# Kernel optimization log

Hardware: AMD Instinct MI355X
Metric: run time of the kernel (lower is better)

## Reference

```python
import jax, jax.numpy as jnp
import numpy as np

N = 100000
C_IN = 128
C_OUT = 128
N_EDGE_TYPE = 7
N_SAMPLES = 2
E = 700000


def setup_inputs() -> dict:
    key = jax.random.key(0)
    k1, k2, k3, k4 = jax.random.split(key, 4)
    x = jax.random.normal(k1, (N, C_IN), dtype=jnp.float32)
    col = jax.random.randint(k2, (E,), 0, N, dtype=jnp.int64)
    # per-edge slot index = row * n_edge_type + edge_type, sorted (select_k_sorted needs sorted idx)
    index_sorted = jnp.sort(jax.random.randint(k3, (E,), 0, N * N_EDGE_TYPE, dtype=jnp.int64))
    weights = jax.random.normal(k4, (N_EDGE_TYPE * C_IN, C_OUT), dtype=jnp.float32)
    return {"x": x, "col": col, "index_sorted": index_sorted, "weights": weights}


def reference(x, col, index_sorted, weights):
    n, c = x.shape
    S = n * N_EDGE_TYPE  # total (node, edge_type) slots
    # group stats over the sorted slot index (replaces unique_consecutive + counts)
    counts = jax.ops.segment_sum(jnp.ones_like(index_sorted, dtype=jnp.int32),
                                 index_sorted, num_segments=S)
    starts = jnp.cumsum(counts) - counts  # first edge position of each slot
    # Monte Carlo: sample N_SAMPLES edges (with replacement) per slot
    rel = jax.random.randint(jax.random.key(42), (S, N_SAMPLES), 0, 1 << 30, dtype=jnp.int32)
    rel = rel % jnp.maximum(counts, 1)[:, None]
    gidx = starts[:, None] + rel              # [S, k] indices into the edge list
    x_col = x[col]                            # [E, C] neighbor features
    gathered = x_col[gidx]                    # [S, k, C]
    gathered = jnp.where((counts > 0)[:, None, None], gathered, jnp.zeros((), x.dtype))
    col_data = gathered.mean(axis=1)          # [S, C]
    # self slot (edge_type = n_edge_type-1) is overwritten with the node's own feature
    self_idx = jnp.arange(n) * N_EDGE_TYPE + (N_EDGE_TYPE - 1)
    col_data = col_data.at[self_idx].set(x)
    return col_data.reshape(n, N_EDGE_TYPE * c) @ weights
```

## Files before the change

kernel.cpp:

```cpp
#include <hip/hip_runtime.h>
#include <hip/hip_bf16.h>
#include <stdint.h>

#define N_NODES 100000
#define C 128
#define NET 7
#define E_EDGES 700000
#define S_SLOTS (N_NODES * NET)
#define BM 64
#define NB_CVTX 6250
#define NB_CVTW 56
#define NB_SCAN ((E_EDGES + 255) / 256)

typedef __attribute__((ext_vector_type(8))) short short8;
typedef __attribute__((ext_vector_type(4))) float f32x4;
typedef __attribute__((ext_vector_type(4))) unsigned int uint4v;

struct TF2 { uint32_t a, b; };

__host__ __device__ constexpr uint32_t rotl32c(uint32_t v, int r) {
    return (v << r) | (v >> (32 - r));
}

__host__ __device__ constexpr TF2 threefry2x32(uint32_t k0, uint32_t k1,
                                               uint32_t x0, uint32_t x1) {
    const uint32_t ks0 = k0, ks1 = k1, ks2 = 0x1BD11BDAu ^ k0 ^ k1;
    x0 += ks0; x1 += ks1;
#define RND(r) { x0 += x1; x1 = rotl32c(x1, (r)); x1 ^= x0; }
    RND(13) RND(15) RND(26) RND(6)
    x0 += ks1; x1 += ks2 + 1u;
    RND(17) RND(29) RND(16) RND(24)
    x0 += ks2; x1 += ks0 + 2u;
    RND(13) RND(15) RND(26) RND(6)
    x0 += ks0; x1 += ks1 + 3u;
    RND(17) RND(29) RND(16) RND(24)
    x0 += ks1; x1 += ks2 + 4u;
    RND(13) RND(15) RND(26) RND(6)
    x0 += ks2; x1 += ks0 + 5u;
#undef RND
    return TF2{x0, x1};
}

constexpr TF2 K2 = threefry2x32(0u, 42u, 0u, 1u);

__device__ __forceinline__ uint32_t jax_bits32(uint32_t f) {
    TF2 o = threefry2x32(K2.a, K2.b, 0u, f);
    return o.a ^ o.b;
}

__device__ __forceinline__ unsigned short f2bf(float f) {
    uint32_t u = __float_as_uint(f);
    u += 0x7fffu + ((u >> 16) & 1u);
    return (unsigned short)(u >> 16);
}

__device__ __forceinline__ uint32_t sumpack(uint32_t a, uint32_t b) {
    float alo = __uint_as_float(a << 16);
    float ahi = __uint_as_float(a & 0xffff0000u);
    float blo = __uint_as_float(b << 16);
    float bhi = __uint_as_float(b & 0xffff0000u);
    return (__float_as_uint(ahi + bhi) & 0xffff0000u) | (__float_as_uint(alo + blo) >> 16);
}

__device__ __forceinline__ uint4v sumpack4(uint4v a, uint4v b) {
    uint4v o;
    o.x = sumpack(a.x, b.x); o.y = sumpack(a.y, b.y);
    o.z = sumpack(a.z, b.z); o.w = sumpack(a.w, b.w);
    return o;
}

__global__ __launch_bounds__(256) void prep(const float* __restrict__ x,
                                            const float* __restrict__ W,
                                            const int* __restrict__ idx,
                                            const int* __restrict__ col,
                                            unsigned short* __restrict__ xb,
                                            unsigned short* __restrict__ Wf,
                                            int2* __restrict__ pairs) {
    const int b = blockIdx.x;
    if (b < NB_CVTX) {
        int i = b * 256 + threadIdx.x;
        const float4* src = (const float4*)x + (size_t)i * 2;
        float4 a = src[0], v = src[1];
        union { unsigned short u[8]; uint4v q; } o;
        o.u[0] = f2bf(a.x); o.u[1] = f2bf(a.y); o.u[2] = f2bf(a.z); o.u[3] = f2bf(a.w);
        o.u[4] = f2bf(v.x); o.u[5] = f2bf(v.y); o.u[6] = f2bf(v.z); o.u[7] = f2bf(v.w);
        ((uint4v*)xb)[i] = o.q;
    } else if (b < NB_CVTX + NB_CVTW) {
        int t = (b - NB_CVTX) * 256 + threadIdx.x;
        int l = t & 63, ks = (t >> 6) & 3, n16 = (t >> 8) & 7, et = t >> 11;
        int n = n16 * 16 + (l & 15);
        int k0 = ks * 32 + (l >> 4) * 8;
        union { unsigned short u[8]; uint4v q; } o;
#pragma unroll
        for (int j = 0; j < 8; j++)
            o.u[j] = f2bf(0.5f * W[(size_t)(et * 128 + k0 + j) * 128 + n]);
        ((uint4v*)Wf)[t] = o.q;
    } else {
        int e = (b - NB_CVTX - NB_CVTW) * 256 + threadIdx.x;
        if (e >= E_EDGES) return;
        int s = idx[e];
        if (e > 0 && idx[e - 1] == s) return;
        if (s % NET == NET - 1) return;
        int len = 1;
        while (e + len < E_EDGES && idx[e + len] == s) ++len;
        uint32_t b0 = jax_bits32((uint32_t)s * 2u + 0u) & 0x3FFFFFFFu;
        uint32_t b1 = jax_bits32((uint32_t)s * 2u + 1u) & 0x3FFFFFFFu;
        int c0 = col[e + (int)(b0 % (uint32_t)len)];
        int c1 = col[e + (int)(b1 % (uint32_t)len)];
        pairs[s] = (c0 == c1) ? make_int2(c0 + 1, 0)
                              : make_int2(c0 + 1, c1 + 1);
    }
}

__global__ __launch_bounds__(512, 4) void fused_mfma(const unsigned short* __restrict__ xb,
                                                     const int2* __restrict__ pairs,
                                                     const unsigned short* __restrict__ Wf,
                                                     float* __restrict__ out) {
    __shared__ unsigned char Alds[2][BM * 256];
    const int tid  = threadIdx.x;
    const int nb   = blockIdx.x * BM;
    const int wave = tid >> 6, lane = tid & 63;
    const int lr   = lane & 15, lg = lane >> 4;
    const char* xbc = (const char*)xb;

    const int srow = tid >> 3;
    const int q16  = (tid & 7) * 16;
    const int arow = nb + srow;
    const int prow = (arow < N_NODES) ? arow * NET : -1;
    const int sa0  = srow * 256 + ((q16 >> 4) ^ (srow & 7)) * 16;
    const int sa1  = sa0 + 128;

    uint4v g0[3][2], g1[3][2];
    int2   pset[3];
    short8 bfr[2][4];

#define GLOAD(SET, PV) { \
    int2 p_ = (PV); pset[SET] = p_; \
    if (p_.x > 0) { \
        const char* b0_ = xbc + ((size_t)(p_.x - 1) << 8); \
        g0[SET][0] = *(const uint4v*)(b0_ + q16); \
        g0[SET][1] = *(const uint4v*)(b0_ + 128 + q16); \
        if (p_.y > 0) { \
            const char* b1_ = xbc + ((size_t)(p_.y - 1) << 8); \
            g1[SET][0] = *(const uint4v*)(b1_ + q16); \
            g1[SET][1] = *(const uint4v*)(b1_ + 128 + q16); \
        } \
    } }

#define COMBINE(SET, BUF) { \
    int2 p_ = pset[SET]; \
    uint4v v0_, v1_; \
    if (p_.x <= 0) { \
        uint4v z_ = {0u, 0u, 0u, 0u}; v0_ = z_; v1_ = z_; \
    } else if (p_.y <= 0) { \
        v0_ = g0[SET][0] + 0x00800080u;    \
        v1_ = g0[SET][1] + 0x00800080u; \
    } else { \
        v0_ = sumpack4(g0[SET][0], g1[SET][0]); \
        v1_ = sumpack4(g0[SET][1], g1[SET][1]); \
    } \
    *(uint4v*)(&Alds[BUF][sa0]) = v0_; \
    *(uint4v*)(&Alds[BUF][sa1]) = v1_; }

#define LOADB(DST, ET) { _Pragma("unroll") \
    for (int ks_ = 0; ks_ < 4; ks_++) \
        (DST)[ks_] = *(const short8*)(Wf \
            + (size_t)((((ET) * 8 + wave) * 4 + ks_) * 512) + lane * 8); }

#define BARRIER() { \
    asm volatile("s_waitcnt lgkmcnt(0)" ::: "memory"); \
    __builtin_amdgcn_s_barrier(); \
    __builtin_amdgcn_sched_barrier(0); }

    f32x4 acc[4];
#pragma unroll
    for (int i = 0; i < 4; i++) acc[i] = (f32x4)0.f;

    int2 pj[7];
#pragma unroll
    for (int j = 0; j < 6; j++)
        pj[j] = (prow >= 0) ? pairs[prow + j] : make_int2(0, 0);
    pj[6] = (prow >= 0) ? make_int2(arow + 1, 0) : make_int2(0, 0);

    GLOAD(0, pj[0])
    GLOAD(1, pj[1])
    GLOAD(2, pj[2])
    LOADB(bfr[0], 0)
    COMBINE(0, 0)
    GLOAD(0, pj[3])
    BARRIER()

#pragma unroll
    for (int et = 0; et < NET; ++et) {
        const int cur = et & 1;

        if (et + 1 < NET) LOADB(bfr[cur ^ 1], et + 1)

        if (et >= 1 && et + 3 < NET) GLOAD(et % 3, pj[et + 3])

        if (et + 1 < NET) COMBINE((et + 1) % 3, cur ^ 1)

        __builtin_amdgcn_s_setprio(1);
#pragma unroll
        for (int ks = 0; ks < 4; ks++) {
            const int coff = (((ks * 4 + lg) ^ (lr & 7)) << 4);
            short8 b_ = bfr[cur][ks];
#pragma unroll
            for (int fm = 0; fm < 4; fm++) {
                short8 a_ = *(const short8*)(&Alds[cur][(fm * 16 + lr) * 256 + coff]);
                acc[fm] = __builtin_amdgcn_mfma_f32_16x16x32_bf16(a_, b_, acc[fm], 0, 0, 0);
            }
        }
        __builtin_amdgcn_s_setprio(0);

        if (et + 1 < NET) BARRIER()
    }

#pragma unroll
    for (int fm = 0; fm < 4; fm++) {
        int row0 = nb + fm * 16 + lg * 4;
        int colo = wave * 16 + lr;
#pragma unroll
        for (int j = 0; j < 4; j++)
            if (row0 + j < N_NODES)
                out[(size_t)(row0 + j) * C + colo] = acc[fm][j];
    }
#undef GLOAD
#undef COMBINE
#undef LOADB
#undef BARRIER
}

extern "C" void kernel_launch(void* const* d_in, const int* in_sizes, int n_in,
                              void* d_out, int out_size, void* d_ws, size_t ws_size,
                              hipStream_t stream) {
    const float* x   = (const float*)d_in[0];
    const int*   col = (const int*)d_in[1];
    const int*   idx = (const int*)d_in[2];
    const float* W   = (const float*)d_in[3];
    float* out = (float*)d_out;

    int2* pairs        = (int2*)d_ws;
    unsigned short* xb = (unsigned short*)((char*)pairs + (size_t)S_SLOTS * 8);
    unsigned short* Wf = xb + (size_t)N_NODES * C;

    hipMemsetAsync(pairs, 0, (size_t)S_SLOTS * sizeof(int2), stream);
    prep<<<NB_CVTX + NB_CVTW + NB_SCAN, 256, 0, stream>>>(x, W, idx, col, xb, Wf, pairs);
    fused_mfma<<<(N_NODES + BM - 1) / BM, 512, 0, stream>>>(xb, pairs, Wf, out);
}
```

Baseline: 77.22 us.

## Drop bf16 pre-conversion of x; gather fp32 rows and convert in fused kernel

Removes the prep pass that converted x to a bf16 copy. The fused kernel now gathers fp32 neighbor rows directly and sums and packs them to bf16 in registers before storing to LDS. This saves a full read and write pass over x, about 51MB of traffic plus 25MB of bf16 writes. In exchange each gather moves twice the bytes, and the per-thread registers for prefetched rows double, which may reduce occupancy.

```diff
diff --git a/kernel.cpp b/kernel.cpp
--- a/kernel.cpp
+++ b/kernel.cpp
@@ -8,7 +8,6 @@
 #define E_EDGES 700000
 #define S_SLOTS (N_NODES * NET)
 #define BM 64
-#define NB_CVTX 6250
 #define NB_CVTW 56
 #define NB_SCAN ((E_EDGES + 255) / 256)
 
@@ -54,39 +53,33 @@
     return (unsigned short)(u >> 16);
 }
 
-__device__ __forceinline__ uint32_t sumpack(uint32_t a, uint32_t b) {
-    float alo = __uint_as_float(a << 16);
-    float ahi = __uint_as_float(a & 0xffff0000u);
-    float blo = __uint_as_float(b << 16);
-    float bhi = __uint_as_float(b & 0xffff0000u);
-    return (__float_as_uint(ahi + bhi) & 0xffff0000u) | (__float_as_uint(alo + blo) >> 16);
-}
-
-__device__ __forceinline__ uint4v sumpack4(uint4v a, uint4v b) {
+__device__ __forceinline__ uint32_t pk(float lo, float hi) {
+    return (__float_as_uint(hi) & 0xffff0000u) | (__float_as_uint(lo) >> 16);
+}
+
+__device__ __forceinline__ uint4v packsum(f32x4 a0, f32x4 a1, f32x4 b0, f32x4 b1) {
+    f32x4 s0 = a0 + b0, s1 = a1 + b1;
     uint4v o;
-    o.x = sumpack(a.x, b.x); o.y = sumpack(a.y, b.y);
-    o.z = sumpack(a.z, b.z); o.w = sumpack(a.w, b.w);
+    o.x = pk(s0.x, s0.y); o.y = pk(s0.z, s0.w);
+    o.z = pk(s1.x, s1.y); o.w = pk(s1.z, s1.w);
     return o;
 }
 
-__global__ __launch_bounds__(256) void prep(const float* __restrict__ x,
-                                            const float* __restrict__ W,
+__device__ __forceinline__ uint4v packone(f32x4 a0, f32x4 a1) {
+    uint4v o;
+    o.x = pk(a0.x, a0.y); o.y = pk(a0.z, a0.w);
+    o.z = pk(a1.x, a1.y); o.w = pk(a1.z, a1.w);
+    return o + 0x00800080u;
+}
+
+__global__ __launch_bounds__(256) void prep(const float* __restrict__ W,
                                             const int* __restrict__ idx,
                                             const int* __restrict__ col,
-                                            unsigned short* __restrict__ xb,
                                             unsigned short* __restrict__ Wf,
                                             int2* __restrict__ pairs) {
     const int b = blockIdx.x;
-    if (b < NB_CVTX) {
-        int i = b * 256 + threadIdx.x;
-        const float4* src = (const float4*)x + (size_t)i * 2;
-        float4 a = src[0], v = src[1];
-        union { unsigned short u[8]; uint4v q; } o;
-        o.u[0] = f2bf(a.x); o.u[1] = f2bf(a.y); o.u[2] = f2bf(a.z); o.u[3] = f2bf(a.w);
-        o.u[4] = f2bf(v.x); o.u[5] = f2bf(v.y); o.u[6] = f2bf(v.z); o.u[7] = f2bf(v.w);
-        ((uint4v*)xb)[i] = o.q;
-    } else if (b < NB_CVTX + NB_CVTW) {
-        int t = (b - NB_CVTX) * 256 + threadIdx.x;
+    if (b < NB_CVTW) {
+        int t = b * 256 + threadIdx.x;
         int l = t & 63, ks = (t >> 6) & 3, n16 = (t >> 8) & 7, et = t >> 11;
         int n = n16 * 16 + (l & 15);
         int k0 = ks * 32 + (l >> 4) * 8;
@@ -96,7 +89,7 @@
             o.u[j] = f2bf(0.5f * W[(size_t)(et * 128 + k0 + j) * 128 + n]);
         ((uint4v*)Wf)[t] = o.q;
     } else {
-        int e = (b - NB_CVTX - NB_CVTW) * 256 + threadIdx.x;
+        int e = (b - NB_CVTW) * 256 + threadIdx.x;
         if (e >= E_EDGES) return;
         int s = idx[e];
         if (e > 0 && idx[e - 1] == s) return;
@@ -112,7 +105,7 @@
     }
 }
 
-__global__ __launch_bounds__(512, 4) void fused_mfma(const unsigned short* __restrict__ xb,
+__global__ __launch_bounds__(512, 4) void fused_mfma(const float* __restrict__ x,
                                                      const int2* __restrict__ pairs,
                                                      const unsigned short* __restrict__ Wf,
                                                      float* __restrict__ out) {
@@ -121,29 +114,33 @@
     const int nb   = blockIdx.x * BM;
     const int wave = tid >> 6, lane = tid & 63;
     const int lr   = lane & 15, lg = lane >> 4;
-    const char* xbc = (const char*)xb;
+    const char* xfc = (const char*)x;
 
     const int srow = tid >> 3;
-    const int q16  = (tid & 7) * 16;
+    const int q32  = (tid & 7) * 32;
     const int arow = nb + srow;
     const int prow = (arow < N_NODES) ? arow * NET : -1;
-    const int sa0  = srow * 256 + ((q16 >> 4) ^ (srow & 7)) * 16;
+    const int sa0  = srow * 256 + (((tid & 7)) ^ (srow & 7)) * 16;
     const int sa1  = sa0 + 128;
 
-    uint4v g0[3][2], g1[3][2];
+    f32x4 g0[3][4], g1[3][4];
     int2   pset[3];
     short8 bfr[2][4];
 
 #define GLOAD(SET, PV) { \
     int2 p_ = (PV); pset[SET] = p_; \
     if (p_.x > 0) { \
-        const char* b0_ = xbc + ((size_t)(p_.x - 1) << 8); \
-        g0[SET][0] = *(const uint4v*)(b0_ + q16); \
-        g0[SET][1] = *(const uint4v*)(b0_ + 128 + q16); \
+        const char* b0_ = xfc + ((size_t)(p_.x - 1) << 9) + q32; \
+        g0[SET][0] = *(const f32x4*)(b0_); \
+        g0[SET][1] = *(const f32x4*)(b0_ + 16); \
+        g0[SET][2] = *(const f32x4*)(b0_ + 256); \
+        g0[SET][3] = *(const f32x4*)(b0_ + 272); \
         if (p_.y > 0) { \
-            const char* b1_ = xbc + ((size_t)(p_.y - 1) << 8); \
-            g1[SET][0] = *(const uint4v*)(b1_ + q16); \
-            g1[SET][1] = *(const uint4v*)(b1_ + 128 + q16); \
+            const char* b1_ = xfc + ((size_t)(p_.y - 1) << 9) + q32; \
+            g1[SET][0] = *(const f32x4*)(b1_); \
+            g1[SET][1] = *(const f32x4*)(b1_ + 16); \
+            g1[SET][2] = *(const f32x4*)(b1_ + 256); \
+            g1[SET][3] = *(const f32x4*)(b1_ + 272); \
         } \
     } }
 
@@ -153,11 +150,11 @@
     if (p_.x <= 0) { \
         uint4v z_ = {0u, 0u, 0u, 0u}; v0_ = z_; v1_ = z_; \
     } else if (p_.y <= 0) { \
-        v0_ = g0[SET][0] + 0x00800080u;    \
-        v1_ = g0[SET][1] + 0x00800080u; \
+        v0_ = packone(g0[SET][0], g0[SET][1]); \
+        v1_ = packone(g0[SET][2], g0[SET][3]); \
     } else { \
-        v0_ = sumpack4(g0[SET][0], g1[SET][0]); \
-        v1_ = sumpack4(g0[SET][1], g1[SET][1]); \
+        v0_ = packsum(g0[SET][0], g0[SET][1], g1[SET][0], g1[SET][1]); \
+        v1_ = packsum(g0[SET][2], g0[SET][3], g1[SET][2], g1[SET][3]); \
     } \
     *(uint4v*)(&Alds[BUF][sa0]) = v0_; \
     *(uint4v*)(&Alds[BUF][sa1]) = v1_; }
@@ -241,10 +238,9 @@
     float* out = (float*)d_out;
 
     int2* pairs        = (int2*)d_ws;
-    unsigned short* xb = (unsigned short*)((char*)pairs + (size_t)S_SLOTS * 8);
-    unsigned short* Wf = xb + (size_t)N_NODES * C;
+    unsigned short* Wf = (unsigned short*)((char*)pairs + (size_t)S_SLOTS * 8);
 
     hipMemsetAsync(pairs, 0, (size_t)S_SLOTS * sizeof(int2), stream);
-    prep<<<NB_CVTX + NB_CVTW + NB_SCAN, 256, 0, stream>>>(x, W, idx, col, xb, Wf, pairs);
-    fused_mfma<<<(N_NODES + BM - 1) / BM, 512, 0, stream>>>(xb, pairs, Wf, out);
-}
+    prep<<<NB_CVTW + NB_SCAN, 256, 0, stream>>>(W, idx, col, Wf, pairs);
+    fused_mfma<<<(N_NODES + BM - 1) / BM, 512, 0, stream>>>(x, pairs, Wf, out);
+}
```

Measured after the change: 179.6 us. 133% more time.

## Shrink row tile to 32 with 256-thread blocks and per-wave 2x2 MFMA tiles

Applied to the files above, without the earlier changes.

Halves the block row tile to 32 nodes and the block to 4 waves, each wave now computing a 32x32 output tile (2 row x 2 column fragments) instead of 64x16. Weight fragments are loaded inside the compute loop per edge type rather than double-buffered one stage ahead, which lowers register use so more blocks fit per CU. The goal is more resident blocks and smaller LDS per block to hide gather latency, at the cost of twice as many blocks, more weight reloads per output row, and no prefetch of B fragments.

```diff
diff --git a/kernel.cpp b/kernel.cpp
--- a/kernel.cpp
+++ b/kernel.cpp
@@ -7,7 +7,7 @@
 #define NET 7
 #define E_EDGES 700000
 #define S_SLOTS (N_NODES * NET)
-#define BM 64
+#define BM 32
 #define NB_CVTX 6250
 #define NB_CVTW 56
 #define NB_SCAN ((E_EDGES + 255) / 256)
@@ -112,7 +112,7 @@
     }
 }
 
-__global__ __launch_bounds__(512, 4) void fused_mfma(const unsigned short* __restrict__ xb,
+__global__ __launch_bounds__(256, 8) void fused_mfma(const unsigned short* __restrict__ xb,
                                                      const int2* __restrict__ pairs,
                                                      const unsigned short* __restrict__ Wf,
                                                      float* __restrict__ out) {
@@ -132,7 +132,6 @@
 
     uint4v g0[3][2], g1[3][2];
     int2   pset[3];
-    short8 bfr[2][4];
 
 #define GLOAD(SET, PV) { \
     int2 p_ = (PV); pset[SET] = p_; \
@@ -162,19 +161,16 @@
     *(uint4v*)(&Alds[BUF][sa0]) = v0_; \
     *(uint4v*)(&Alds[BUF][sa1]) = v1_; }
 
-#define LOADB(DST, ET) { _Pragma("unroll") \
-    for (int ks_ = 0; ks_ < 4; ks_++) \
-        (DST)[ks_] = *(const short8*)(Wf \
-            + (size_t)((((ET) * 8 + wave) * 4 + ks_) * 512) + lane * 8); }
-
 #define BARRIER() { \
     asm volatile("s_waitcnt lgkmcnt(0)" ::: "memory"); \
     __builtin_amdgcn_s_barrier(); \
     __builtin_amdgcn_sched_barrier(0); }
 
-    f32x4 acc[4];
-#pragma unroll
-    for (int i = 0; i < 4; i++) acc[i] = (f32x4)0.f;
+    f32x4 acc[2][2];
+#pragma unroll
+    for (int i = 0; i < 2; i++)
+#pragma unroll
+        for (int j = 0; j < 2; j++) acc[i][j] = (f32x4)0.f;
 
     int2 pj[7];
 #pragma unroll
@@ -185,7 +181,6 @@
     GLOAD(0, pj[0])
     GLOAD(1, pj[1])
     GLOAD(2, pj[2])
-    LOADB(bfr[0], 0)
     COMBINE(0, 0)
     GLOAD(0, pj[3])
     BARRIER()
@@ -194,21 +189,27 @@
     for (int et = 0; et < NET; ++et) {
         const int cur = et & 1;
 
-        if (et + 1 < NET) LOADB(bfr[cur ^ 1], et + 1)
-
         if (et >= 1 && et + 3 < NET) GLOAD(et % 3, pj[et + 3])
 
         if (et + 1 < NET) COMBINE((et + 1) % 3, cur ^ 1)
 
         __builtin_amdgcn_s_setprio(1);
 #pragma unroll
-        for (int ks = 0; ks < 4; ks++) {
-            const int coff = (((ks * 4 + lg) ^ (lr & 7)) << 4);
-            short8 b_ = bfr[cur][ks];
-#pragma unroll
-            for (int fm = 0; fm < 4; fm++) {
-                short8 a_ = *(const short8*)(&Alds[cur][(fm * 16 + lr) * 256 + coff]);
-                acc[fm] = __builtin_amdgcn_mfma_f32_16x16x32_bf16(a_, b_, acc[fm], 0, 0, 0);
+        for (int fn = 0; fn < 2; fn++) {
+            short8 bq[4];
+#pragma unroll
+            for (int ks = 0; ks < 4; ks++)
+                bq[ks] = *(const short8*)(Wf
+                    + (size_t)(((et * 8 + wave * 2 + fn) * 4 + ks) * 512) + lane * 8);
+#pragma unroll
+            for (int ks = 0; ks < 4; ks++) {
+                const int coff = (((ks * 4 + lg) ^ (lr & 7)) << 4);
+#pragma unroll
+                for (int fm = 0; fm < 2; fm++) {
+                    short8 a_ = *(const short8*)(&Alds[cur][(fm * 16 + lr) * 256 + coff]);
+                    acc[fm][fn] = __builtin_amdgcn_mfma_f32_16x16x32_bf16(
+                        a_, bq[ks], acc[fm][fn], 0, 0, 0);
+                }
             }
         }
         __builtin_amdgcn_s_setprio(0);
@@ -217,17 +218,19 @@
     }
 
 #pragma unroll
-    for (int fm = 0; fm < 4; fm++) {
+    for (int fm = 0; fm < 2; fm++) {
         int row0 = nb + fm * 16 + lg * 4;
-        int colo = wave * 16 + lr;
-#pragma unroll
-        for (int j = 0; j < 4; j++)
-            if (row0 + j < N_NODES)
-                out[(size_t)(row0 + j) * C + colo] = acc[fm][j];
+#pragma unroll
+        for (int fn = 0; fn < 2; fn++) {
+            int colo = wave * 32 + fn * 16 + lr;
+#pragma unroll
+            for (int j = 0; j < 4; j++)
+                if (row0 + j < N_NODES)
+                    out[(size_t)(row0 + j) * C + colo] = acc[fm][fn][j];
+        }
     }
 #undef GLOAD
 #undef COMBINE
-#undef LOADB
 #undef BARRIER
 }
 
@@ -246,5 +249,5 @@
 
     hipMemsetAsync(pairs, 0, (size_t)S_SLOTS * sizeof(int2), stream);
     prep<<<NB_CVTX + NB_CVTW + NB_SCAN, 256, 0, stream>>>(x, W, idx, col, xb, Wf, pairs);
-    fused_mfma<<<(N_NODES + BM - 1) / BM, 512, 0, stream>>>(xb, pairs, Wf, out);
-}
+    fused_mfma<<<(N_NODES + BM - 1) / BM, 256, 0, stream>>>(xb, pairs, Wf, out);
+}
```

Result: slower. 137.1 us (+77.5%).
